# Performance work log

Hardware: AMD Instinct MI355X
Metric: run time of the kernel (lower is better)

## Reference

```python
import jax, jax.numpy as jnp
import numpy as np

K = 10          # hardcoded in module (self.K = 10)
H = 26          # neighbors per query point in this run
PAD_H = 28      # layer_ind2neighbor[layer_ind=0]
KP_EXTENT = 1.2 # linear-influence extent


def setup_inputs() -> dict:
    key = jax.random.key(0)
    ks = jax.random.split(key, 6)
    N, Ns, Cin, Cout = 65536, 65536, 64, 128
    q_pts = jax.random.normal(ks[0], (N, 3), jnp.float32)
    s_pts = jax.random.normal(ks[1], (Ns, 3), jnp.float32)
    neighb_inds = jax.random.randint(ks[2], (N, H), 0, Ns)
    x = jax.random.normal(ks[3], (Ns, Cin), jnp.float32)
    # kernel_points_generator: Linear(PAD_H*3 -> K*3)
    gen_W = jax.random.normal(ks[4], (K * 3, PAD_H * 3), jnp.float32) * (1.0 / np.sqrt(PAD_H * 3))
    gen_b = jnp.zeros((K * 3,), jnp.float32)
    # KPConv weights: [K, in, out] (kaiming_uniform in torch; scaled normal here)
    weights = jax.random.normal(ks[5], (K, Cin, Cout), jnp.float32) * (1.0 / np.sqrt(Cin))
    return {"q_pts": q_pts, "s_pts": s_pts, "x": x,
            "gen_W": gen_W, "gen_b": gen_b, "weights": weights,
            "neighb_inds": neighb_inds}


def _kpconv(q_pts, s_pts, x, gen_W, gen_b, weights, neighb_inds):
    N = q_pts.shape[0]
    # shadow support point far away (index Ns)
    s_pad = jnp.concatenate([s_pts, jnp.full((1, 3), 1e6, s_pts.dtype)], axis=0)
    neighbors = s_pad[neighb_inds] - q_pts[:, None, :]                          # [N,H,3]
    # generative kernel points: pad neighbor list with -1 up to PAD_H, run linear
    padded = jnp.concatenate(
        [neighbors, jnp.full((N, PAD_H - H, 3), -1.0, neighbors.dtype)], axis=1)
    kp = (padded.reshape(N, -1) @ gen_W.T + gen_b).reshape(N, 1, K, 3)          # [N,1,K,3]
    diff = neighbors[:, :, None, :] - kp                                        # [N,H,K,3]
    sq_d = jnp.sum(diff * diff, axis=3)                                         # [N,H,K]
    # KP_influence == 'linear'
    all_w = jnp.maximum(1.0 - jnp.sqrt(sq_d) / KP_EXTENT, 0.0)
    all_w = jnp.swapaxes(all_w, 1, 2)                                           # [N,K,H]
    # shadow feature row (zeros) at index Ns
    x_pad = jnp.concatenate([x, jnp.zeros((1, x.shape[1]), x.dtype)], axis=0)
    neighb_x = x_pad[neighb_inds]                                               # [N,H,Cin]
    weighted = jnp.einsum('nkh,nhi->nki', all_w, neighb_x)                      # [N,K,Cin]
    return jnp.einsum('nki,kio->no', weighted, weights)                         # [N,Cout]


def reference(q_pts, s_pts, x, gen_W, gen_b, weights, neighb_inds):
    return _kpconv(q_pts, s_pts, x, gen_W, gen_b, weights, neighb_inds)
```

## Files before the change

kernel.cpp:

```cpp
#include <hip/hip_runtime.h>
#include <stdint.h>

#define N_Q   65536
#define N_S   65536
#define NB_H  26
#define PAD_H 28
#define KP    10
#define CIN   64
#define COUT  128
#define MT    16
#define BM    16

typedef unsigned short u16x8  __attribute__((ext_vector_type(8)));
typedef float          f32x4  __attribute__((ext_vector_type(4)));
typedef _Float16       f16x8  __attribute__((ext_vector_type(8)));
typedef _Float16       f16x2  __attribute__((ext_vector_type(2)));
typedef unsigned int   u32x4  __attribute__((ext_vector_type(4)));
typedef unsigned int   u32x2  __attribute__((ext_vector_type(2)));

#define CVT_BLOCKS 2049
#define PACK_BLOCKS 40

static __device__ __forceinline__ unsigned short f2h(float f) {
  return __builtin_bit_cast(unsigned short, (_Float16)f);
}

static __device__ __forceinline__ unsigned int pkrtz_u32(float a, float b) {
  return __builtin_bit_cast(unsigned int, __builtin_amdgcn_cvt_pkrtz(a, b));
}

static __device__ __forceinline__ float fdot2u(unsigned int a, unsigned int b, float c) {
#if __has_builtin(__builtin_amdgcn_fdot2)
  return __builtin_amdgcn_fdot2(__builtin_bit_cast(f16x2, a),
                                __builtin_bit_cast(f16x2, b), c, false);
#else
  f16x2 ha = __builtin_bit_cast(f16x2, a), hb = __builtin_bit_cast(f16x2, b);
  return c + (float)ha[0] * (float)hb[0] + (float)ha[1] * (float)hb[1];
#endif
}

__global__ void prep_kernel(const float* __restrict__ x,
                            const float* __restrict__ w,
                            unsigned short* __restrict__ xh,
                            unsigned short* __restrict__ bp) {
  if (blockIdx.x < CVT_BLOCKS) {
    long t = (long)blockIdx.x * blockDim.x + threadIdx.x;
    long off = t * 8;
    if (off >= (long)(N_S + 1) * CIN) return;
    u16x8 o;
    if (off < (long)N_S * CIN) {
      f32x4 a = *(const f32x4*)(x + off);
      f32x4 b = *(const f32x4*)(x + off + 4);
      o[0] = f2h(a[0]); o[1] = f2h(a[1]); o[2] = f2h(a[2]); o[3] = f2h(a[3]);
      o[4] = f2h(b[0]); o[5] = f2h(b[1]); o[6] = f2h(b[2]); o[7] = f2h(b[3]);
    } else {
      o = (u16x8)0;
    }
    *(u16x8*)(xh + off) = o;
  } else {
    int t = (blockIdx.x - CVT_BLOCKS) * blockDim.x + threadIdx.x;
    if (t >= 8 * 20 * 64) return;
    int lane = t & 63;
    int frag = t >> 6;
    int ks = frag % 20;
    int ct = frag / 20;
    int row0 = ks * 32 + (lane >> 4) * 8;
    int col  = ct * 16 + (lane & 15);
    u16x8 o;
    #pragma unroll
    for (int j = 0; j < 8; ++j) o[j] = f2h(w[(row0 + j) * COUT + col]);
    *(u16x8*)(bp + (long)t * 8) = o;
  }
}

__global__ void __launch_bounds__(256, 4)
kpconv_fused(const float* __restrict__ q_pts, const float* __restrict__ s_pts,
             const float* __restrict__ gen_W, const float* __restrict__ gen_b,
             const int* __restrict__ inds, const unsigned short* __restrict__ xh,
             const unsigned short* __restrict__ bp, float* __restrict__ out) {

  __shared__ int            sh_ind[MT][NB_H];
  __shared__ float          sh_nbr[MT][80];
  __shared__ float          sh_kp[MT][KP * 3];
  __shared__ unsigned int   sh_aw[MT][13][12];
  __shared__ unsigned short sA[20 * 512];

  const int  tid  = threadIdx.x;
  const long row0 = (long)blockIdx.x * BM;

  for (int it = tid; it < MT * NB_H; it += 256) {
    int m = it / NB_H, h = it % NB_H;
    int n = (int)row0 + m;
    int ind = inds[n * NB_H + h];
    sh_ind[m][h] = ind;
    float sx, sy, sz;
    if ((unsigned)ind < (unsigned)N_S) {
      sx = s_pts[ind * 3 + 0]; sy = s_pts[ind * 3 + 1]; sz = s_pts[ind * 3 + 2];
    } else {
      sx = 1e6f; sy = 1e6f; sz = 1e6f;
    }
    sh_nbr[m][h * 3 + 0] = sx - q_pts[n * 3 + 0];
    sh_nbr[m][h * 3 + 1] = sy - q_pts[n * 3 + 1];
    sh_nbr[m][h * 3 + 2] = sz - q_pts[n * 3 + 2];
  }
  if (tid < MT * 2) sh_nbr[tid >> 1][78 + (tid & 1)] = -1.0f;
  __syncthreads();

  for (int it = tid; it < MT * KP * 3; it += 256) {
    int m = it / 30, r = it % 30;
    const float* Wr = gen_W + r * (PAD_H * 3);
    const f32x4* W4 = (const f32x4*)Wr;
    const f32x4* N4 = (const f32x4*)&sh_nbr[m][0];
    f32x4 accv = {0.f, 0.f, 0.f, 0.f};
    #pragma unroll
    for (int j = 0; j < 20; ++j) accv += W4[j] * N4[j];
    sh_kp[m][r] = gen_b[r] - (Wr[80] + Wr[81] + Wr[82] + Wr[83])
                + accv[0] + accv[1] + accv[2] + accv[3];
  }
  __syncthreads();

  for (int p = tid; p < MT * 13 * KP; p += 256) {
    int k = p % KP;
    int t = p / KP;
    int m = t & (MT - 1);
    int hp = t >> 4;
    float kx = sh_kp[m][k * 3 + 0], ky = sh_kp[m][k * 3 + 1], kz = sh_kp[m][k * 3 + 2];
    int h0 = hp * 2;
    float dx0 = sh_nbr[m][h0 * 3 + 0] - kx;
    float dy0 = sh_nbr[m][h0 * 3 + 1] - ky;
    float dz0 = sh_nbr[m][h0 * 3 + 2] - kz;
    float w0 = fmaxf(1.0f - sqrtf(dx0 * dx0 + dy0 * dy0 + dz0 * dz0) * (1.0f / 1.2f), 0.0f);
    float dx1 = sh_nbr[m][h0 * 3 + 3] - kx;
    float dy1 = sh_nbr[m][h0 * 3 + 4] - ky;
    float dz1 = sh_nbr[m][h0 * 3 + 5] - kz;
    float w1 = fmaxf(1.0f - sqrtf(dx1 * dx1 + dy1 * dy1 + dz1 * dz1) * (1.0f / 1.2f), 0.0f);
    sh_aw[m][hp][k] = pkrtz_u32(w0, w1);
  }
  __syncthreads();

  {
    const int g  = tid >> 5;
    const int l  = tid & 31;
    const int i0 = l * 2;
    const int rA = g, rB = g + 8;

    float a0A[KP], a1A[KP], a0B[KP], a1B[KP];
    #pragma unroll
    for (int k = 0; k < KP; ++k) { a0A[k] = 0.f; a1A[k] = 0.f; a0B[k] = 0.f; a1B[k] = 0.f; }

    unsigned int xrA[8], xrB[8];
    #pragma unroll
    for (int h = 0; h < 8; ++h) {
      xrA[h] = *(const unsigned int*)(xh + (long)sh_ind[rA][h] * CIN + i0);
      xrB[h] = *(const unsigned int*)(xh + (long)sh_ind[rB][h] * CIN + i0);
    }

    #pragma unroll
    for (int p = 0; p < 13; ++p) {
      unsigned int r0A = xrA[(2 * p) & 7], r1A = xrA[(2 * p + 1) & 7];
      unsigned int r0B = xrB[(2 * p) & 7], r1B = xrB[(2 * p + 1) & 7];
      if (2 * p + 8 < NB_H) {
        xrA[(2 * p) & 7] = *(const unsigned int*)(xh + (long)sh_ind[rA][2 * p + 8] * CIN + i0);
        xrB[(2 * p) & 7] = *(const unsigned int*)(xh + (long)sh_ind[rB][2 * p + 8] * CIN + i0);
      }
      if (2 * p + 9 < NB_H) {
        xrA[(2 * p + 1) & 7] = *(const unsigned int*)(xh + (long)sh_ind[rA][2 * p + 9] * CIN + i0);
        xrB[(2 * p + 1) & 7] = *(const unsigned int*)(xh + (long)sh_ind[rB][2 * p + 9] * CIN + i0);
      }
      unsigned int p0A = __builtin_amdgcn_perm(r1A, r0A, 0x05040100u);
      unsigned int p1A = __builtin_amdgcn_perm(r1A, r0A, 0x07060302u);
      unsigned int p0B = __builtin_amdgcn_perm(r1B, r0B, 0x05040100u);
      unsigned int p1B = __builtin_amdgcn_perm(r1B, r0B, 0x07060302u);

      unsigned int wA[KP], wB[KP];
      *(u32x4*)&wA[0] = *(const u32x4*)&sh_aw[rA][p][0];
      *(u32x4*)&wA[4] = *(const u32x4*)&sh_aw[rA][p][4];
      *(u32x2*)&wA[8] = *(const u32x2*)&sh_aw[rA][p][8];
      *(u32x4*)&wB[0] = *(const u32x4*)&sh_aw[rB][p][0];
      *(u32x4*)&wB[4] = *(const u32x4*)&sh_aw[rB][p][4];
      *(u32x2*)&wB[8] = *(const u32x2*)&sh_aw[rB][p][8];

      #pragma unroll
      for (int k = 0; k < KP; ++k) {
        a0A[k] = fdot2u(wA[k], p0A, a0A[k]);
        a1A[k] = fdot2u(wA[k], p1A, a1A[k]);
        a0B[k] = fdot2u(wB[k], p0B, a0B[k]);
        a1B[k] = fdot2u(wB[k], p1B, a1B[k]);
      }
    }

    const int kq  = (l & 15) >> 2;
    const int qhi = l >> 4;
    const int j2  = (2 * l) & 7;
    const int swz = (kq << 3) ^ (qhi << 5);
    const int hbA = (((kq * 16 + rA) * 8 + j2) ^ swz) + qhi * 512;
    const int hbB = (((kq * 16 + rB) * 8 + j2) ^ swz) + qhi * 512;
    #pragma unroll
    for (int k = 0; k < KP; ++k) {
      *(unsigned int*)(sA + k * 1024 + hbA) = pkrtz_u32(a0A[k], a1A[k]);
      *(unsigned int*)(sA + k * 1024 + hbB) = pkrtz_u32(a0B[k], a1B[k]);
    }
  }
  __syncthreads();

  {
    const int wave = tid >> 6;
    const int lane = tid & 63;
    const int ct0  = wave * 2, ct1 = ct0 + 1;
    const int a0   = (lane * 8) ^ ((lane >> 4) << 3);

    f32x4 acc[2];
    acc[0] = (f32x4){0.f, 0.f, 0.f, 0.f};
    acc[1] = (f32x4){0.f, 0.f, 0.f, 0.f};

    u16x8 pb0[4], pb1[4];
    #pragma unroll
    for (int d = 0; d < 4; ++d) {
      pb0[d] = *(const u16x8*)(bp + (long)((ct0 * 20 + d) * 64 + lane) * 8);
      pb1[d] = *(const u16x8*)(bp + (long)((ct1 * 20 + d) * 64 + lane) * 8);
    }

    #pragma unroll
    for (int ks = 0; ks < 20; ++ks) {
      f16x8 b0 = __builtin_bit_cast(f16x8, pb0[ks & 3]);
      f16x8 b1 = __builtin_bit_cast(f16x8, pb1[ks & 3]);
      if (ks + 4 < 20) {
        pb0[ks & 3] = *(const u16x8*)(bp + (long)((ct0 * 20 + ks + 4) * 64 + lane) * 8);
        pb1[ks & 3] = *(const u16x8*)(bp + (long)((ct1 * 20 + ks + 4) * 64 + lane) * 8);
      }
      u16x8 au = *(const u16x8*)&sA[ks * 512 + (a0 ^ ((ks & 1) << 5))];
      f16x8 a = __builtin_bit_cast(f16x8, au);
      acc[0] = __builtin_amdgcn_mfma_f32_16x16x32_f16(a, b0, acc[0], 0, 0, 0);
      acc[1] = __builtin_amdgcn_mfma_f32_16x16x32_f16(a, b1, acc[1], 0, 0, 0);
    }

    const int col   = lane & 15;
    const int rbase = (lane >> 4) * 4;
    #pragma unroll
    for (int r = 0; r < 4; ++r) {
      long row = row0 + rbase + r;
      __builtin_nontemporal_store(acc[0][r], &out[row * COUT + ct0 * 16 + col]);
      __builtin_nontemporal_store(acc[1][r], &out[row * COUT + ct1 * 16 + col]);
    }
  }
}

extern "C" void kernel_launch(void* const* d_in, const int* in_sizes, int n_in,
                              void* d_out, int out_size, void* d_ws, size_t ws_size,
                              hipStream_t stream) {
  const float* q_pts = (const float*)d_in[0];
  const float* s_pts = (const float*)d_in[1];
  const float* x     = (const float*)d_in[2];
  const float* gen_W = (const float*)d_in[3];
  const float* gen_b = (const float*)d_in[4];
  const float* wts   = (const float*)d_in[5];
  const int*   inds  = (const int*)d_in[6];
  float* out = (float*)d_out;

  unsigned short* xh = (unsigned short*)d_ws;
  unsigned short* bp = xh + (size_t)(N_S + 1) * CIN;

  prep_kernel<<<CVT_BLOCKS + PACK_BLOCKS, 256, 0, stream>>>(x, wts, xh, bp);
  kpconv_fused<<<N_Q / BM, 256, 0, stream>>>(q_pts, s_pts, gen_W, gen_b,
                                             inds, xh, bp, out);
}
```

Measured before the change: 175.7 us.

## Compute per-point weighted neighbor aggregation with MFMA instead of fdot2

Replaces the VALU fdot2 loop that aggregated neighbor features by kernel-point weights with a per-point 16x16x32 f16 MFMA. Kernel weights are staged in a zero-padded fragment layout and features are gathered per element. The first-stage shared buffers are aliased into one raw region reused for the second GEMM's A tile, with a new swizzle. The aim is to move the dominant aggregation FLOPs onto matrix cores. In exchange, feature gathers become 16-bit scalar loads, per-element f16 stores to shared memory are added, and padding adds wasted MFMA work.

```diff
diff --git a/kernel.cpp b/kernel.cpp
--- a/kernel.cpp
+++ b/kernel.cpp
@@ -14,9 +14,7 @@
 typedef unsigned short u16x8  __attribute__((ext_vector_type(8)));
 typedef float          f32x4  __attribute__((ext_vector_type(4)));
 typedef _Float16       f16x8  __attribute__((ext_vector_type(8)));
-typedef _Float16       f16x2  __attribute__((ext_vector_type(2)));
 typedef unsigned int   u32x4  __attribute__((ext_vector_type(4)));
-typedef unsigned int   u32x2  __attribute__((ext_vector_type(2)));
 
 #define CVT_BLOCKS 2049
 #define PACK_BLOCKS 40
@@ -27,16 +25,6 @@
 
 static __device__ __forceinline__ unsigned int pkrtz_u32(float a, float b) {
   return __builtin_bit_cast(unsigned int, __builtin_amdgcn_cvt_pkrtz(a, b));
-}
-
-static __device__ __forceinline__ float fdot2u(unsigned int a, unsigned int b, float c) {
-#if __has_builtin(__builtin_amdgcn_fdot2)
-  return __builtin_amdgcn_fdot2(__builtin_bit_cast(f16x2, a),
-                                __builtin_bit_cast(f16x2, b), c, false);
-#else
-  f16x2 ha = __builtin_bit_cast(f16x2, a), hb = __builtin_bit_cast(f16x2, b);
-  return c + (float)ha[0] * (float)hb[0] + (float)ha[1] * (float)hb[1];
-#endif
 }
 
 __global__ void prep_kernel(const float* __restrict__ x,
@@ -73,20 +61,29 @@
   }
 }
 
+#define SH_NBR(m, c) (((float*)smem_raw)[(m) * 80 + (c)])
+#define SH_KP(m, r)  (((float*)(smem_raw + 5120))[(m) * 30 + (r)])
+
 __global__ void __launch_bounds__(256, 4)
 kpconv_fused(const float* __restrict__ q_pts, const float* __restrict__ s_pts,
              const float* __restrict__ gen_W, const float* __restrict__ gen_b,
              const int* __restrict__ inds, const unsigned short* __restrict__ xh,
              const unsigned short* __restrict__ bp, float* __restrict__ out) {
 
+  __shared__ char           smem_raw[20480] __attribute__((aligned(16)));
+  __shared__ unsigned short wfrag[16 * 512] __attribute__((aligned(16)));
   __shared__ int            sh_ind[MT][NB_H];
-  __shared__ float          sh_nbr[MT][80];
-  __shared__ float          sh_kp[MT][KP * 3];
-  __shared__ unsigned int   sh_aw[MT][13][12];
-  __shared__ unsigned short sA[20 * 512];
+
+  unsigned short* sA = (unsigned short*)smem_raw;
 
   const int  tid  = threadIdx.x;
   const long row0 = (long)blockIdx.x * BM;
+
+  {
+    unsigned int* wz = (unsigned int*)wfrag;
+    #pragma unroll
+    for (int i = 0; i < 16; ++i) wz[tid + 256 * i] = 0u;
+  }
 
   for (int it = tid; it < MT * NB_H; it += 256) {
     int m = it / NB_H, h = it % NB_H;
@@ -99,22 +96,22 @@
     } else {
       sx = 1e6f; sy = 1e6f; sz = 1e6f;
     }
-    sh_nbr[m][h * 3 + 0] = sx - q_pts[n * 3 + 0];
-    sh_nbr[m][h * 3 + 1] = sy - q_pts[n * 3 + 1];
-    sh_nbr[m][h * 3 + 2] = sz - q_pts[n * 3 + 2];
-  }
-  if (tid < MT * 2) sh_nbr[tid >> 1][78 + (tid & 1)] = -1.0f;
+    SH_NBR(m, h * 3 + 0) = sx - q_pts[n * 3 + 0];
+    SH_NBR(m, h * 3 + 1) = sy - q_pts[n * 3 + 1];
+    SH_NBR(m, h * 3 + 2) = sz - q_pts[n * 3 + 2];
+  }
+  if (tid < MT * 2) SH_NBR(tid >> 1, 78 + (tid & 1)) = -1.0f;
   __syncthreads();
 
   for (int it = tid; it < MT * KP * 3; it += 256) {
     int m = it / 30, r = it % 30;
     const float* Wr = gen_W + r * (PAD_H * 3);
     const f32x4* W4 = (const f32x4*)Wr;
-    const f32x4* N4 = (const f32x4*)&sh_nbr[m][0];
+    const f32x4* N4 = (const f32x4*)((float*)smem_raw + m * 80);
     f32x4 accv = {0.f, 0.f, 0.f, 0.f};
     #pragma unroll
     for (int j = 0; j < 20; ++j) accv += W4[j] * N4[j];
-    sh_kp[m][r] = gen_b[r] - (Wr[80] + Wr[81] + Wr[82] + Wr[83])
+    SH_KP(m, r) = gen_b[r] - (Wr[80] + Wr[81] + Wr[82] + Wr[83])
                 + accv[0] + accv[1] + accv[2] + accv[3];
   }
   __syncthreads();
@@ -124,82 +121,80 @@
     int t = p / KP;
     int m = t & (MT - 1);
     int hp = t >> 4;
-    float kx = sh_kp[m][k * 3 + 0], ky = sh_kp[m][k * 3 + 1], kz = sh_kp[m][k * 3 + 2];
+    float kx = SH_KP(m, k * 3 + 0), ky = SH_KP(m, k * 3 + 1), kz = SH_KP(m, k * 3 + 2);
     int h0 = hp * 2;
-    float dx0 = sh_nbr[m][h0 * 3 + 0] - kx;
-    float dy0 = sh_nbr[m][h0 * 3 + 1] - ky;
-    float dz0 = sh_nbr[m][h0 * 3 + 2] - kz;
+    float dx0 = SH_NBR(m, h0 * 3 + 0) - kx;
+    float dy0 = SH_NBR(m, h0 * 3 + 1) - ky;
+    float dz0 = SH_NBR(m, h0 * 3 + 2) - kz;
     float w0 = fmaxf(1.0f - sqrtf(dx0 * dx0 + dy0 * dy0 + dz0 * dz0) * (1.0f / 1.2f), 0.0f);
-    float dx1 = sh_nbr[m][h0 * 3 + 3] - kx;
-    float dy1 = sh_nbr[m][h0 * 3 + 4] - ky;
-    float dz1 = sh_nbr[m][h0 * 3 + 5] - kz;
+    float dx1 = SH_NBR(m, h0 * 3 + 3) - kx;
+    float dy1 = SH_NBR(m, h0 * 3 + 4) - ky;
+    float dz1 = SH_NBR(m, h0 * 3 + 5) - kz;
     float w1 = fmaxf(1.0f - sqrtf(dx1 * dx1 + dy1 * dy1 + dz1 * dz1) * (1.0f / 1.2f), 0.0f);
-    sh_aw[m][hp][k] = pkrtz_u32(w0, w1);
+    *(unsigned int*)(wfrag + m * 512 + (h0 >> 3) * 128 + k * 8 + (h0 & 7)) =
+        pkrtz_u32(w0, w1);
   }
   __syncthreads();
 
   {
-    const int g  = tid >> 5;
-    const int l  = tid & 31;
-    const int i0 = l * 2;
-    const int rA = g, rB = g + 8;
-
-    float a0A[KP], a1A[KP], a0B[KP], a1B[KP];
-    #pragma unroll
-    for (int k = 0; k < KP; ++k) { a0A[k] = 0.f; a1A[k] = 0.f; a0B[k] = 0.f; a1B[k] = 0.f; }
-
-    unsigned int xrA[8], xrB[8];
-    #pragma unroll
-    for (int h = 0; h < 8; ++h) {
-      xrA[h] = *(const unsigned int*)(xh + (long)sh_ind[rA][h] * CIN + i0);
-      xrB[h] = *(const unsigned int*)(xh + (long)sh_ind[rB][h] * CIN + i0);
-    }
-
-    #pragma unroll
-    for (int p = 0; p < 13; ++p) {
-      unsigned int r0A = xrA[(2 * p) & 7], r1A = xrA[(2 * p + 1) & 7];
-      unsigned int r0B = xrB[(2 * p) & 7], r1B = xrB[(2 * p + 1) & 7];
-      if (2 * p + 8 < NB_H) {
-        xrA[(2 * p) & 7] = *(const unsigned int*)(xh + (long)sh_ind[rA][2 * p + 8] * CIN + i0);
-        xrB[(2 * p) & 7] = *(const unsigned int*)(xh + (long)sh_ind[rB][2 * p + 8] * CIN + i0);
-      }
-      if (2 * p + 9 < NB_H) {
-        xrA[(2 * p + 1) & 7] = *(const unsigned int*)(xh + (long)sh_ind[rA][2 * p + 9] * CIN + i0);
-        xrB[(2 * p + 1) & 7] = *(const unsigned int*)(xh + (long)sh_ind[rB][2 * p + 9] * CIN + i0);
-      }
-      unsigned int p0A = __builtin_amdgcn_perm(r1A, r0A, 0x05040100u);
-      unsigned int p1A = __builtin_amdgcn_perm(r1A, r0A, 0x07060302u);
-      unsigned int p0B = __builtin_amdgcn_perm(r1B, r0B, 0x05040100u);
-      unsigned int p1B = __builtin_amdgcn_perm(r1B, r0B, 0x07060302u);
-
-      unsigned int wA[KP], wB[KP];
-      *(u32x4*)&wA[0] = *(const u32x4*)&sh_aw[rA][p][0];
-      *(u32x4*)&wA[4] = *(const u32x4*)&sh_aw[rA][p][4];
-      *(u32x2*)&wA[8] = *(const u32x2*)&sh_aw[rA][p][8];
-      *(u32x4*)&wB[0] = *(const u32x4*)&sh_aw[rB][p][0];
-      *(u32x4*)&wB[4] = *(const u32x4*)&sh_aw[rB][p][4];
-      *(u32x2*)&wB[8] = *(const u32x2*)&sh_aw[rB][p][8];
-
-      #pragma unroll
-      for (int k = 0; k < KP; ++k) {
-        a0A[k] = fdot2u(wA[k], p0A, a0A[k]);
-        a1A[k] = fdot2u(wA[k], p1A, a1A[k]);
-        a0B[k] = fdot2u(wB[k], p0B, a0B[k]);
-        a1B[k] = fdot2u(wB[k], p1B, a1B[k]);
-      }
-    }
-
-    const int kq  = (l & 15) >> 2;
-    const int qhi = l >> 4;
-    const int j2  = (2 * l) & 7;
-    const int swz = (kq << 3) ^ (qhi << 5);
-    const int hbA = (((kq * 16 + rA) * 8 + j2) ^ swz) + qhi * 512;
-    const int hbB = (((kq * 16 + rB) * 8 + j2) ^ swz) + qhi * 512;
-    #pragma unroll
-    for (int k = 0; k < KP; ++k) {
-      *(unsigned int*)(sA + k * 1024 + hbA) = pkrtz_u32(a0A[k], a1A[k]);
-      *(unsigned int*)(sA + k * 1024 + hbB) = pkrtz_u32(a0B[k], a1B[k]);
-    }
+    const int lane = tid & 63;
+    const int wv   = tid >> 6;
+    const int g    = lane >> 4;
+    const int cl   = lane & 15;
+    const unsigned short* xbase = xh + cl;
+
+#define LOADM(MM, V)                                                          \
+    {                                                                         \
+      _Pragma("unroll")                                                       \
+      for (int j = 0; j < 8; ++j) {                                           \
+        int h = g * 8 + j;                                                    \
+        int ind = sh_ind[MM][h < NB_H ? h : 0];                               \
+        const unsigned short* pj = xbase + (long)ind * CIN;                   \
+        _Pragma("unroll")                                                     \
+        for (int ct = 0; ct < 4; ++ct) V[ct][j] = pj[ct * 16];                \
+      }                                                                       \
+    }
+
+#define CONSUME(MM, V)                                                        \
+    {                                                                         \
+      u16x8 afr = *(const u16x8*)&wfrag[(MM) * 512 + (g * 16 + cl) * 8];      \
+      f16x8 a = __builtin_bit_cast(f16x8, afr);                               \
+      _Pragma("unroll")                                                       \
+      for (int ct = 0; ct < 4; ++ct) {                                        \
+        u32x4 bu;                                                             \
+        bu[0] = V[ct][0] | (V[ct][1] << 16);                                  \
+        bu[1] = V[ct][2] | (V[ct][3] << 16);                                  \
+        bu[2] = V[ct][4] | (V[ct][5] << 16);                                  \
+        bu[3] = V[ct][6] | (V[ct][7] << 16);                                  \
+        f16x8 b = __builtin_bit_cast(f16x8, bu);                              \
+        f32x4 d = __builtin_amdgcn_mfma_f32_16x16x32_f16(                     \
+            a, b, (f32x4){0.f, 0.f, 0.f, 0.f}, 0, 0, 0);                      \
+        const int e   = ((ct & 1) << 4) | cl;                                 \
+        const int sj  = ((e >> 3) * 128) + (MM) * 8 + (e & 7);                \
+        const int ct2 = ct >> 1;                                              \
+        _Pragma("unroll")                                                     \
+        for (int r = 0; r < 4; ++r) {                                         \
+          int k = g * 4 + r;                                                  \
+          if (k < KP) {                                                       \
+            int ks = k * 2 + ct2;                                             \
+            sA[ks * 512 + (sj ^ (((ks >> 3) & 3) << 4))] = f2h(d[r]);         \
+          }                                                                   \
+        }                                                                     \
+      }                                                                       \
+    }
+
+    unsigned int v0[4][8], v1[4][8];
+    const int m0 = wv * 4;
+    LOADM(m0, v0)
+    LOADM(m0 + 1, v1)
+    CONSUME(m0, v0)
+    LOADM(m0 + 2, v0)
+    CONSUME(m0 + 1, v1)
+    LOADM(m0 + 3, v1)
+    CONSUME(m0 + 2, v0)
+    CONSUME(m0 + 3, v1)
+#undef LOADM
+#undef CONSUME
   }
   __syncthreads();
 
@@ -207,7 +202,6 @@
     const int wave = tid >> 6;
     const int lane = tid & 63;
     const int ct0  = wave * 2, ct1 = ct0 + 1;
-    const int a0   = (lane * 8) ^ ((lane >> 4) << 3);
 
     f32x4 acc[2];
     acc[0] = (f32x4){0.f, 0.f, 0.f, 0.f};
@@ -228,7 +222,8 @@
         pb0[ks & 3] = *(const u16x8*)(bp + (long)((ct0 * 20 + ks + 4) * 64 + lane) * 8);
         pb1[ks & 3] = *(const u16x8*)(bp + (long)((ct1 * 20 + ks + 4) * 64 + lane) * 8);
       }
-      u16x8 au = *(const u16x8*)&sA[ks * 512 + (a0 ^ ((ks & 1) << 5))];
+      const int swzk = ((ks >> 3) & 3) << 4;
+      u16x8 au = *(const u16x8*)&sA[ks * 512 + ((lane * 8) ^ swzk)];
       f16x8 a = __builtin_bit_cast(f16x8, au);
       acc[0] = __builtin_amdgcn_mfma_f32_16x16x32_f16(a, b0, acc[0], 0, 0, 0);
       acc[1] = __builtin_amdgcn_mfma_f32_16x16x32_f16(a, b1, acc[1], 0, 0, 0);
```

Result: slower. 179.3 us (+2.1%).

## Make each wave own four query rows and drop block barriers in prologue

Applied to the files above, without the earlier changes.

Each wave now handles its own four query rows through neighbor gathering, kernel-point generation and influence weights, so three block-wide __syncthreads are replaced by s_waitcnt lgkmcnt(0) fences inside the wave. Feature gathers for the weighted-sum stage and the first MFMA B-operand loads are issued earlier, so their latency overlaps the weight computation and the one remaining barrier. Correctness now depends on the LDS data being produced and consumed within the same wave. Relying on waitcnt instead of a barrier is fragile if the compiler reorders the LDS accesses.

```diff
diff --git a/kernel.cpp b/kernel.cpp
--- a/kernel.cpp
+++ b/kernel.cpp
@@ -86,74 +86,89 @@
   __shared__ unsigned short sA[20 * 512];
 
   const int  tid  = threadIdx.x;
+  const int  lane = tid & 63;
+  const int  wv   = tid >> 6;
+  const int  m0   = wv * 4;
   const long row0 = (long)blockIdx.x * BM;
 
-  for (int it = tid; it < MT * NB_H; it += 256) {
-    int m = it / NB_H, h = it % NB_H;
-    int n = (int)row0 + m;
-    int ind = inds[n * NB_H + h];
-    sh_ind[m][h] = ind;
-    float sx, sy, sz;
-    if ((unsigned)ind < (unsigned)N_S) {
-      sx = s_pts[ind * 3 + 0]; sy = s_pts[ind * 3 + 1]; sz = s_pts[ind * 3 + 2];
-    } else {
-      sx = 1e6f; sy = 1e6f; sz = 1e6f;
-    }
-    sh_nbr[m][h * 3 + 0] = sx - q_pts[n * 3 + 0];
-    sh_nbr[m][h * 3 + 1] = sy - q_pts[n * 3 + 1];
-    sh_nbr[m][h * 3 + 2] = sz - q_pts[n * 3 + 2];
-  }
-  if (tid < MT * 2) sh_nbr[tid >> 1][78 + (tid & 1)] = -1.0f;
-  __syncthreads();
-
-  for (int it = tid; it < MT * KP * 3; it += 256) {
-    int m = it / 30, r = it % 30;
-    const float* Wr = gen_W + r * (PAD_H * 3);
-    const f32x4* W4 = (const f32x4*)Wr;
-    const f32x4* N4 = (const f32x4*)&sh_nbr[m][0];
-    f32x4 accv = {0.f, 0.f, 0.f, 0.f};
-    #pragma unroll
-    for (int j = 0; j < 20; ++j) accv += W4[j] * N4[j];
-    sh_kp[m][r] = gen_b[r] - (Wr[80] + Wr[81] + Wr[82] + Wr[83])
-                + accv[0] + accv[1] + accv[2] + accv[3];
-  }
-  __syncthreads();
-
-  for (int p = tid; p < MT * 13 * KP; p += 256) {
-    int k = p % KP;
-    int t = p / KP;
-    int m = t & (MT - 1);
-    int hp = t >> 4;
-    float kx = sh_kp[m][k * 3 + 0], ky = sh_kp[m][k * 3 + 1], kz = sh_kp[m][k * 3 + 2];
-    int h0 = hp * 2;
-    float dx0 = sh_nbr[m][h0 * 3 + 0] - kx;
-    float dy0 = sh_nbr[m][h0 * 3 + 1] - ky;
-    float dz0 = sh_nbr[m][h0 * 3 + 2] - kz;
-    float w0 = fmaxf(1.0f - sqrtf(dx0 * dx0 + dy0 * dy0 + dz0 * dz0) * (1.0f / 1.2f), 0.0f);
-    float dx1 = sh_nbr[m][h0 * 3 + 3] - kx;
-    float dy1 = sh_nbr[m][h0 * 3 + 4] - ky;
-    float dz1 = sh_nbr[m][h0 * 3 + 5] - kz;
-    float w1 = fmaxf(1.0f - sqrtf(dx1 * dx1 + dy1 * dy1 + dz1 * dz1) * (1.0f / 1.2f), 0.0f);
-    sh_aw[m][hp][k] = pkrtz_u32(w0, w1);
-  }
-  __syncthreads();
+  #pragma unroll
+  for (int it = 0; it < 2; ++it) {
+    int idx = it * 64 + lane;
+    if (idx < 4 * NB_H) {
+      int m = m0 + idx / NB_H;
+      int h = idx % NB_H;
+      int n = (int)row0 + m;
+      int ind = inds[n * NB_H + h];
+      sh_ind[m][h] = ind;
+      float sx, sy, sz;
+      if ((unsigned)ind < (unsigned)N_S) {
+        sx = s_pts[ind * 3 + 0]; sy = s_pts[ind * 3 + 1]; sz = s_pts[ind * 3 + 2];
+      } else {
+        sx = 1e6f; sy = 1e6f; sz = 1e6f;
+      }
+      sh_nbr[m][h * 3 + 0] = sx - q_pts[n * 3 + 0];
+      sh_nbr[m][h * 3 + 1] = sy - q_pts[n * 3 + 1];
+      sh_nbr[m][h * 3 + 2] = sz - q_pts[n * 3 + 2];
+    }
+  }
+  if (lane < 8) sh_nbr[m0 + (lane >> 1)][78 + (lane & 1)] = -1.0f;
+  asm volatile("s_waitcnt lgkmcnt(0)" ::: "memory");
+
+  const int il = lane & 31;
+  const int g2 = lane >> 5;
+  const int i0 = il * 2;
+  const int rA = m0 + g2, rB = rA + 2;
+  unsigned int xrA[8], xrB[8];
+  #pragma unroll
+  for (int h = 0; h < 8; ++h) {
+    xrA[h] = *(const unsigned int*)(xh + (long)sh_ind[rA][h] * CIN + i0);
+    xrB[h] = *(const unsigned int*)(xh + (long)sh_ind[rB][h] * CIN + i0);
+  }
+
+  #pragma unroll
+  for (int it = 0; it < 2; ++it) {
+    int idx = it * 64 + lane;
+    if (idx < 4 * 30) {
+      int m = m0 + idx / 30;
+      int r = idx % 30;
+      const float* Wr = gen_W + r * (PAD_H * 3);
+      const f32x4* W4 = (const f32x4*)Wr;
+      const f32x4* N4 = (const f32x4*)&sh_nbr[m][0];
+      f32x4 accv = {0.f, 0.f, 0.f, 0.f};
+      #pragma unroll
+      for (int j = 0; j < 20; ++j) accv += W4[j] * N4[j];
+      sh_kp[m][r] = gen_b[r] - (Wr[80] + Wr[81] + Wr[82] + Wr[83])
+                  + accv[0] + accv[1] + accv[2] + accv[3];
+    }
+  }
+  asm volatile("s_waitcnt lgkmcnt(0)" ::: "memory");
+
+  for (int it = 0; it < 9; ++it) {
+    int idx = it * 64 + lane;
+    if (idx < 4 * 13 * KP) {
+      int k  = idx % KP;
+      int t  = idx / KP;
+      int m  = m0 + (t & 3);
+      int hp = t >> 2;
+      float kx = sh_kp[m][k * 3 + 0], ky = sh_kp[m][k * 3 + 1], kz = sh_kp[m][k * 3 + 2];
+      int h0 = hp * 2;
+      float dx0 = sh_nbr[m][h0 * 3 + 0] - kx;
+      float dy0 = sh_nbr[m][h0 * 3 + 1] - ky;
+      float dz0 = sh_nbr[m][h0 * 3 + 2] - kz;
+      float w0 = fmaxf(1.0f - sqrtf(dx0 * dx0 + dy0 * dy0 + dz0 * dz0) * (1.0f / 1.2f), 0.0f);
+      float dx1 = sh_nbr[m][h0 * 3 + 3] - kx;
+      float dy1 = sh_nbr[m][h0 * 3 + 4] - ky;
+      float dz1 = sh_nbr[m][h0 * 3 + 5] - kz;
+      float w1 = fmaxf(1.0f - sqrtf(dx1 * dx1 + dy1 * dy1 + dz1 * dz1) * (1.0f / 1.2f), 0.0f);
+      sh_aw[m][hp][k] = pkrtz_u32(w0, w1);
+    }
+  }
+  asm volatile("s_waitcnt lgkmcnt(0)" ::: "memory");
 
   {
-    const int g  = tid >> 5;
-    const int l  = tid & 31;
-    const int i0 = l * 2;
-    const int rA = g, rB = g + 8;
-
     float a0A[KP], a1A[KP], a0B[KP], a1B[KP];
     #pragma unroll
     for (int k = 0; k < KP; ++k) { a0A[k] = 0.f; a1A[k] = 0.f; a0B[k] = 0.f; a1B[k] = 0.f; }
-
-    unsigned int xrA[8], xrB[8];
-    #pragma unroll
-    for (int h = 0; h < 8; ++h) {
-      xrA[h] = *(const unsigned int*)(xh + (long)sh_ind[rA][h] * CIN + i0);
-      xrB[h] = *(const unsigned int*)(xh + (long)sh_ind[rB][h] * CIN + i0);
-    }
 
     #pragma unroll
     for (int p = 0; p < 13; ++p) {
@@ -189,9 +204,9 @@
       }
     }
 
-    const int kq  = (l & 15) >> 2;
-    const int qhi = l >> 4;
-    const int j2  = (2 * l) & 7;
+    const int kq  = (il & 15) >> 2;
+    const int qhi = il >> 4;
+    const int j2  = (2 * il) & 7;
     const int swz = (kq << 3) ^ (qhi << 5);
     const int hbA = (((kq * 16 + rA) * 8 + j2) ^ swz) + qhi * 512;
     const int hbB = (((kq * 16 + rB) * 8 + j2) ^ swz) + qhi * 512;
@@ -201,24 +216,23 @@
       *(unsigned int*)(sA + k * 1024 + hbB) = pkrtz_u32(a0B[k], a1B[k]);
     }
   }
+
+  const int ct0 = wv * 2, ct1 = ct0 + 1;
+  u16x8 pb0[4], pb1[4];
+  #pragma unroll
+  for (int d = 0; d < 4; ++d) {
+    pb0[d] = *(const u16x8*)(bp + (long)((ct0 * 20 + d) * 64 + lane) * 8);
+    pb1[d] = *(const u16x8*)(bp + (long)((ct1 * 20 + d) * 64 + lane) * 8);
+  }
+
   __syncthreads();
 
   {
-    const int wave = tid >> 6;
-    const int lane = tid & 63;
-    const int ct0  = wave * 2, ct1 = ct0 + 1;
-    const int a0   = (lane * 8) ^ ((lane >> 4) << 3);
+    const int a0 = (lane * 8) ^ ((lane >> 4) << 3);
 
     f32x4 acc[2];
     acc[0] = (f32x4){0.f, 0.f, 0.f, 0.f};
     acc[1] = (f32x4){0.f, 0.f, 0.f, 0.f};
-
-    u16x8 pb0[4], pb1[4];
-    #pragma unroll
-    for (int d = 0; d < 4; ++d) {
-      pb0[d] = *(const u16x8*)(bp + (long)((ct0 * 20 + d) * 64 + lane) * 8);
-      pb1[d] = *(const u16x8*)(bp + (long)((ct1 * 20 + d) * 64 + lane) * 8);
-    }
 
     #pragma unroll
     for (int ks = 0; ks < 20; ++ks) {
```

After: 169.9 us. 3.3% less time.
